# Performance work log

Hardware: AMD Instinct MI355X
Metric: run time of the kernel (lower is better)

The kernel has to match this reference:

```python
import jax, jax.numpy as jnp
import numpy as np

IMG = 1024.0            # image H = W
PRE_NMS, POST_NMS = 2000, 1000
NMS_THR, MIN_SZ = 0.7, 16.0
B = 16                  # batch of images


def _make_anchors():
    # Standard FPN anchor tiling: strides {4..64}, one scale per level, 3 ratios.
    strides = [4, 8, 16, 32, 64]
    scales = [32.0, 64.0, 128.0, 256.0, 512.0]
    ratios = [0.5, 1.0, 2.0]
    out = []
    for s, sc in zip(strides, scales):
        n = int(IMG) // s
        c = (np.arange(n, dtype=np.float32) + 0.5) * s
        xs, ys = np.meshgrid(c, c, indexing="xy")
        ctr = np.stack([xs.ravel(), ys.ravel()], -1)              # (n*n, 2) cx,cy
        wh = np.array([[sc * np.sqrt(1.0 / r), sc * np.sqrt(r)] for r in ratios],
                      dtype=np.float32)                           # (3, 2)
        b = np.concatenate([ctr[:, None, :] - wh[None] / 2,
                            ctr[:, None, :] + wh[None] / 2], -1)  # (n*n, 3, 4)
        out.append(b.reshape(-1, 4))
    return np.concatenate(out, 0).astype(np.float32)              # (261888, 4)


def setup_inputs() -> dict:
    key = jax.random.key(0)
    k1, k2 = jax.random.split(key)
    anchors = jnp.asarray(_make_anchors())
    A = anchors.shape[0]
    deltas = jax.random.normal(k1, (B, A, 4), dtype=jnp.float32) * 0.1
    scores = jax.random.uniform(k2, (B, A), dtype=jnp.float32)    # post-sigmoid objectness
    return {"anchors": anchors, "deltas": deltas, "scores": scores}


def _decode(anchors, deltas):
    # decode_boxes: deltas (tx,ty,tw,th) applied to anchors; dw/dh clamped at 4.0
    aw = anchors[:, 2] - anchors[:, 0]
    ah = anchors[:, 3] - anchors[:, 1]
    ax = anchors[:, 0] + 0.5 * aw
    ay = anchors[:, 1] + 0.5 * ah
    dx, dy = deltas[..., 0], deltas[..., 1]
    dw = jnp.minimum(deltas[..., 2], 4.0)
    dh = jnp.minimum(deltas[..., 3], 4.0)
    px = dx * aw + ax
    py = dy * ah + ay
    pw = jnp.exp(dw) * aw
    ph = jnp.exp(dh) * ah
    return jnp.stack([px - 0.5 * pw, py - 0.5 * ph,
                      px + 0.5 * pw, py + 0.5 * ph], -1)


def _box_iou(a, b):
    area_a = (a[:, 2] - a[:, 0]) * (a[:, 3] - a[:, 1])
    area_b = (b[:, 2] - b[:, 0]) * (b[:, 3] - b[:, 1])
    lt = jnp.maximum(a[:, None, :2], b[None, :, :2])
    rb = jnp.minimum(a[:, None, 2:], b[None, :, 2:])
    wh = jnp.clip(rb - lt, 0.0)
    inter = wh[..., 0] * wh[..., 1]
    return inter / (area_a[:, None] + area_b[None, :] - inter + 1e-6)


def _filter_one(props, s):
    # RegionProposalNetwork._filter: clip -> size filter -> topk(pre_nms) -> NMS -> post_nms
    x1 = jnp.clip(props[:, 0], 0.0, IMG)
    y1 = jnp.clip(props[:, 1], 0.0, IMG)
    x2 = jnp.clip(props[:, 2], 0.0, IMG)
    y2 = jnp.clip(props[:, 3], 0.0, IMG)
    valid = (x2 - x1 >= MIN_SZ) & (y2 - y1 >= MIN_SZ)
    ms = jnp.where(valid, s, -jnp.inf)                 # mask instead of boolean gather (jit)
    vals, idx = jax.lax.top_k(ms, PRE_NMS)            # sorted desc, as in scores.topk
    b = jnp.stack([x1, y1, x2, y2], -1)[idx]          # (PRE_NMS, 4)
    iou = _box_iou(b, b)                              # (PRE_NMS, PRE_NMS)
    later = jnp.arange(PRE_NMS)

    def body(i, keep):
        # suppress later boxes overlapping a still-kept box i (greedy NMS)
        sup = (iou[i] > NMS_THR) & keep[i] & (later > i)
        return keep & ~sup

    keep = jax.lax.fori_loop(0, PRE_NMS, body, jnp.ones(PRE_NMS, dtype=bool))
    fs = jnp.where(keep, vals, -jnp.inf)
    fv, fi = jax.lax.top_k(fs, POST_NMS)              # kept boxes, desc score order
    good = jnp.isfinite(fv)                           # padding mask for suppressed slots
    boxes = jnp.where(good[:, None], b[fi], 0.0)
    sc = jnp.where(good, fv, 0.0)
    return jnp.concatenate([boxes, sc[:, None]], -1)  # (POST_NMS, 5) = (x1,y1,x2,y2,score)


def reference(anchors, deltas, scores):
    props = _decode(anchors, deltas)                  # (B, A, 4)
    return jax.vmap(_filter_one)(props, scores)       # (B, POST_NMS, 5)
```

## Files before the change

kernel.cpp:

```cpp
#include <hip/hip_runtime.h>
#include <stdint.h>
#include <math.h>


#define IMGF 1024.0f
#define PRE_NMS 2000
#define POST_NMS 1000
#define NMS_THR 0.7f
#define MIN_SZ 16.0f
#define CAP 4096
#define SEL 2048
#define NW (SEL / 64)
#define CNT_STRIDE 32
#define KEY_NEGINF 0x007FFFFFu
#define MAXCHUNK 12

__device__ __forceinline__ uint32_t f2key(float f) {
  uint32_t u = __float_as_uint(f);
  return (u & 0x80000000u) ? ~u : (u | 0x80000000u);
}
__device__ __forceinline__ float key2f(uint32_t k) {
  uint32_t u = (k & 0x80000000u) ? (k & 0x7FFFFFFFu) : ~k;
  return __uint_as_float(u);
}

__device__ __forceinline__ unsigned long long readlane_u64(unsigned long long v,
                                                           int lane) {
  unsigned int lo = __builtin_amdgcn_readlane((unsigned int)v, lane);
  unsigned int hi = __builtin_amdgcn_readlane((unsigned int)(v >> 32), lane);
  return ((unsigned long long)hi << 32) | lo;
}

__device__ __forceinline__ float4 decode_clip(float4 anc, float4 dlt) {
  float aw = anc.z - anc.x;
  float ah = anc.w - anc.y;
  float ax = anc.x + 0.5f * aw;
  float ay = anc.y + 0.5f * ah;
  float dw = fminf(dlt.z, 4.0f);
  float dh = fminf(dlt.w, 4.0f);
  float px = dlt.x * aw + ax;
  float py = dlt.y * ah + ay;
  float pw = expf(dw) * aw;
  float ph = expf(dh) * ah;
  float x1 = px - 0.5f * pw, y1 = py - 0.5f * ph;
  float x2 = px + 0.5f * pw, y2 = py + 0.5f * ph;
  x1 = fminf(fmaxf(x1, 0.0f), IMGF);
  y1 = fminf(fmaxf(y1, 0.0f), IMGF);
  x2 = fminf(fmaxf(x2, 0.0f), IMGF);
  y2 = fminf(fmaxf(y2, 0.0f), IMGF);
  return make_float4(x1, y1, x2, y2);
}

__global__ void k_decode(const float4* __restrict__ anchors,
                         const float4* __restrict__ deltas,
                         const float* __restrict__ scores,
                         uint32_t* __restrict__ keys,
                         uint32_t* __restrict__ chist,
                         int A, int chunks) {
  int b = blockIdx.y;
  int t = threadIdx.x;
  int lane = t & 63;
  __shared__ uint32_t shist[256];
  shist[t] = 0;
  __syncthreads();
  int base_a = blockIdx.x * (chunks * 256);
  for (int c = 0; c < chunks; c++) {
    int a = base_a + c * 256 + t;
    bool inb = a < A;
    int ac = inb ? a : (A - 1);
    size_t i = (size_t)b * A + ac;
    float4 box = decode_clip(anchors[ac], deltas[i]);
    bool valid = (box.z - box.x >= MIN_SZ) && (box.w - box.y >= MIN_SZ);
    float ms = valid ? scores[i] : -INFINITY;
    uint32_t k = f2key(ms);
    if (inb) keys[i] = k;
    uint32_t bucket = k >> 24;
    bool fin = inb && (k != KEY_NEGINF);
    unsigned long long match = __ballot(fin);
#pragma unroll
    for (int bit = 0; bit < 8; bit++) {
      bool hb = (bucket >> bit) & 1;
      unsigned long long bb = __ballot(hb && fin);
      match &= hb ? bb : ~bb;
    }
    if (fin && (__ffsll((long long)match) - 1 == lane))
      atomicAdd(&shist[bucket], (uint32_t)__popcll(match));
  }
  __syncthreads();
  uint32_t v = shist[t];
  if (v) atomicAdd(&chist[b * 256 + t], v);
}

__global__ void k_coarse(const uint32_t* __restrict__ chist,
                         int* __restrict__ cbArr,
                         uint32_t* __restrict__ cumArr) {
  int b = blockIdx.x;
  int t = threadIdx.x;
  __shared__ uint32_t sA[256];
  sA[t] = chist[b * 256 + t];
  for (int d = 1; d < 256; d <<= 1) {
    __syncthreads();
    uint32_t v = sA[t] + ((t + d < 256) ? sA[t + d] : 0u);
    __syncthreads();
    sA[t] = v;
  }
  __syncthreads();
  if (t == 0 && sA[0] < PRE_NMS) {
    cbArr[b] = -1;
    cumArr[b] = 0;
  }
  uint32_t nxt = (t < 255) ? sA[t + 1] : 0u;
  if (sA[t] >= PRE_NMS && nxt < PRE_NMS) {
    cbArr[b] = t;
    cumArr[b] = nxt;
  }
}

__global__ void k_fine(const uint32_t* __restrict__ keys,
                       const int* __restrict__ cbArr,
                       uint32_t* __restrict__ fhist,
                       int A, int chunks) {
  int b = blockIdx.y;
  int t = threadIdx.x;
  int cb = cbArr[b];
  if (cb < 0) return;
  __shared__ uint32_t shist[256];
  shist[t] = 0;
  __syncthreads();
  int base_a = blockIdx.x * (chunks * 256);
  uint32_t cbu = (uint32_t)cb;
  for (int c = 0; c < chunks; c++) {
    int a = base_a + c * 256 + t;
    if (a >= A) break;
    uint32_t k = keys[(size_t)b * A + a];
    if ((k >> 24) == cbu && k != KEY_NEGINF)
      atomicAdd(&shist[(k >> 16) & 0xFFu], 1u);
  }
  __syncthreads();
  uint32_t v = shist[t];
  if (v) atomicAdd(&fhist[b * 256 + t], v);
}

__global__ void k_thresh(const uint32_t* __restrict__ fhist,
                         const int* __restrict__ cbArr,
                         const uint32_t* __restrict__ cumArr,
                         uint32_t* __restrict__ thresh,
                         uint32_t* __restrict__ cnts) {
  int b = blockIdx.x;
  int t = threadIdx.x;
  __shared__ uint32_t sA[256];
  if (t < 2) cnts[b * CNT_STRIDE + t] = 0;
  int cb = cbArr[b];
  if (cb < 0) {
    if (t == 0) thresh[b] = 0u;
    return;
  }
  uint32_t cumAbove = cumArr[b];
  sA[t] = fhist[b * 256 + t];
  for (int d = 1; d < 256; d <<= 1) {
    __syncthreads();
    uint32_t v = sA[t] + ((t + d < 256) ? sA[t + d] : 0u);
    __syncthreads();
    sA[t] = v;
  }
  __syncthreads();
  uint32_t nxt = (t < 255) ? sA[t + 1] : 0u;
  if (cumAbove + sA[t] >= PRE_NMS && cumAbove + nxt < PRE_NMS)
    thresh[b] = (uint32_t)((cb << 8) | t);
}

__global__ void k_gather(const uint32_t* __restrict__ keys,
                         const uint32_t* __restrict__ thresh,
                         uint32_t* __restrict__ cnts,
                         unsigned long long* __restrict__ cand_sort,
                         float4* __restrict__ sel_box,
                         float* __restrict__ sel_score,
                         int A, int chunks) {
  int b = blockIdx.y;
  int t = threadIdx.x;
  int lane = t & 63;
  int w = t >> 6;
  if (blockIdx.x < SEL / 256) {
    int r = blockIdx.x * 256 + t;
    sel_score[(size_t)b * SEL + r] = -INFINITY;
    sel_box[(size_t)b * SEL + r] = make_float4(0.0f, 0.0f, 0.0f, 0.0f);
  }
  __shared__ unsigned long long s_mA[MAXCHUNK * 4], s_mT[MAXCHUNK * 4];
  __shared__ uint32_t s_offA[MAXCHUNK * 4], s_offT[MAXCHUNK * 4];
  __shared__ uint32_t s_cA[MAXCHUNK * 4], s_cT[MAXCHUNK * 4];
  __shared__ uint32_t s_baseA, s_baseT;
  uint32_t beta = thresh[b];
  uint32_t kreg[MAXCHUNK];
  int base_a = blockIdx.x * (chunks * 256);
  for (int c = 0; c < chunks; c++) {
    int a = base_a + c * 256 + t;
    bool inb = a < A;
    uint32_t k = inb ? keys[(size_t)b * A + a] : KEY_NEGINF;
    kreg[c] = k;
    uint32_t bk = k >> 16;
    bool fin = (k != KEY_NEGINF);
    unsigned long long mA = __ballot(fin && (bk > beta));
    unsigned long long mT = __ballot(fin && (bk == beta));
    if (lane == 0) {
      s_mA[c * 4 + w] = mA;
      s_mT[c * 4 + w] = mT;
    }
  }
  __syncthreads();
  if (t < chunks * 4) {
    s_cA[t] = (uint32_t)__popcll(s_mA[t]);
    s_cT[t] = (uint32_t)__popcll(s_mT[t]);
  }
  __syncthreads();
  if (t == 0) {
    uint32_t accA = 0, accT = 0;
    for (int id = 0; id < chunks * 4; id++) {
      s_offA[id] = accA;
      accA += s_cA[id];
      s_offT[id] = accT;
      accT += s_cT[id];
    }
    s_baseA = accA ? atomicAdd(&cnts[b * CNT_STRIDE + 0], accA) : 0u;
    s_baseT = accT ? atomicAdd(&cnts[b * CNT_STRIDE + 1], accT) : 0u;
  }
  __syncthreads();
  uint32_t baseA = s_baseA, baseT = s_baseT;
  unsigned long long lower = ((unsigned long long)1 << lane) - 1;
  for (int c = 0; c < chunks; c++) {
    int id = c * 4 + w;
    unsigned long long mA = s_mA[id], mT = s_mT[id];
    bool above = (mA >> lane) & 1;
    bool tie = (mT >> lane) & 1;
    if (!(above || tie)) continue;
    int pos;
    if (above) {
      pos = (int)(baseA + s_offA[id] + (uint32_t)__popcll(mA & lower));
      if (pos >= PRE_NMS) continue;
    } else {
      pos = CAP - 1 - (int)(baseT + s_offT[id] + (uint32_t)__popcll(mT & lower));
      if (pos < PRE_NMS) continue;
    }
    int a = base_a + c * 256 + t;
    cand_sort[(size_t)b * CAP + pos] =
        ((unsigned long long)kreg[c] << 32) | (uint32_t)(~(uint32_t)a);
  }
}

__global__ void k_rank(const unsigned long long* __restrict__ cand_sort,
                       const uint32_t* __restrict__ cnts,
                       const float4* __restrict__ anchors,
                       const float4* __restrict__ deltas,
                       float4* __restrict__ sel_box,
                       float* __restrict__ sel_score, int A) {
  int b = blockIdx.y;
  int t = threadIdx.x;
  uint32_t c1 = cnts[b * CNT_STRIDE + 0];
  if (c1 > PRE_NMS) c1 = PRE_NMS;
  uint32_t c2 = cnts[b * CNT_STRIDE + 1];
  if (c2 > CAP - PRE_NMS) c2 = CAP - PRE_NMS;
  int loTie = CAP - (int)c2;
  int bs = blockIdx.x * 256;
  if (bs >= (int)c1 && bs + 256 <= loTie) return;
  int s = bs + t;
  bool live = (s < (int)c1) || (s >= loTie);
  unsigned long long myKey = live ? cand_sort[(size_t)b * CAP + s] : 0ull;
  __shared__ unsigned long long tile[256];
  int rank = 0;
  for (int ts = 0; ts < CAP; ts += 256) {
    if (ts >= (int)c1 && ts + 256 <= loTie) continue;
    int idx = ts + t;
    bool lv = (idx < (int)c1) || (idx >= loTie);
    __syncthreads();
    tile[t] = lv ? cand_sort[(size_t)b * CAP + idx] : 0ull;
    __syncthreads();
    if (live) {
#pragma unroll 8
      for (int j = 0; j < 256; j++) rank += (tile[j] > myKey) ? 1 : 0;
    }
  }
  if (live && rank < SEL) {
    uint32_t a = ~((uint32_t)myKey);
    float4 box = decode_clip(anchors[a], deltas[(size_t)b * A + a]);
    sel_score[(size_t)b * SEL + rank] = key2f((uint32_t)(myKey >> 32));
    sel_box[(size_t)b * SEL + rank] = box;
  }
}

__global__ void k_nmsmask(const float4* __restrict__ sel_box,
                          unsigned long long* __restrict__ mask,
                          unsigned long long* __restrict__ maskT) {
  int jb = blockIdx.x;
  int ib = blockIdx.y;
  int b = blockIdx.z;
  int t = threadIdx.x;
  int i = ib * 64 + t;
  if (jb < ib) {
    mask[((size_t)b * SEL + i) * NW + jb] = 0ull;
    return;
  }
  __shared__ float4 cb[64];
  __shared__ float careb[64];
  int j0 = jb * 64;
  float4 cbx = sel_box[(size_t)b * SEL + j0 + t];
  cb[t] = cbx;
  careb[t] = (cbx.z - cbx.x) * (cbx.w - cbx.y);
  __syncthreads();
  bool pad = (i >= PRE_NMS);
  if (pad && jb != ib) {
    mask[((size_t)b * SEL + i) * NW + jb] = 0ull;
    return;
  }
  float4 a = sel_box[(size_t)b * SEL + i];
  float area_a = (a.z - a.x) * (a.w - a.y);
  unsigned long long bits = 0ull;
  int jmax = min(64, PRE_NMS - j0);
  if (!pad) {
    for (int jj = 0; jj < jmax; jj++) {
      int j = j0 + jj;
      if (j <= i) continue;
      float4 bb = cb[jj];
      float ltx = fmaxf(a.x, bb.x), lty = fmaxf(a.y, bb.y);
      float rbx = fminf(a.z, bb.z), rby = fminf(a.w, bb.w);
      float w = fmaxf(rbx - ltx, 0.0f), hgt = fmaxf(rby - lty, 0.0f);
      float inter = w * hgt;
      float iou = inter / (area_a + careb[jj] - inter + 1e-6f);
      if (iou > NMS_THR) bits |= (1ull << jj);
    }
  }
  mask[((size_t)b * SEL + i) * NW + jb] = bits;
  if (jb == ib) {
    unsigned long long myT = 0ull;
#pragma unroll 1
    for (int jj = 0; jj < 64; jj++) {
      unsigned long long colw = __ballot((bits >> jj) & 1ull);
      if (t == jj) myT = colw;
    }
    maskT[(size_t)b * SEL + i] = myT;
  }
}

__global__ void __launch_bounds__(64, 1)
k_scanout(const float4* __restrict__ sel_box,
          const float* __restrict__ sel_score,
          const unsigned long long* __restrict__ mask,
          const unsigned long long* __restrict__ maskT,
          float* __restrict__ out) {
  int b = blockIdx.x;
  int t = threadIdx.x;
  int tw = t & 31;
  __shared__ uint32_t keptList[POST_NMS + 64];
  __shared__ unsigned long long tile[2][64 * NW];
  unsigned long long removed = 0ull;
  int kc = 0;
  const unsigned long long* mbase = mask + (size_t)b * SEL * NW;
  const unsigned long long* tbase = maskT + (size_t)b * SEL;
  const int lastChunk = (PRE_NMS - 1) / 64;
  int g = t >> 4;
  int cq = (t & 15) * 16;

  {
    const char* gb = (const char*)mbase;
#pragma unroll
    for (int k = 0; k < 16; k++) {
      const void* gp = gb + (size_t)(4 * k + g) * (NW * 8) + cq;
      __builtin_amdgcn_global_load_lds(
          (const __attribute__((address_space(1))) uint32_t*)gp,
          (__attribute__((address_space(3))) uint32_t*)&tile[0][(size_t)k * 128],
          16, 0, 0);
    }
  }
  unsigned long long colm = tbase[t];
  uint32_t scb = __float_as_uint(sel_score[(size_t)b * SEL + t]);

  for (int chunk = 0; chunk <= lastChunk; chunk++) {
    int cur = chunk & 1;
    unsigned long long colm_n = 0ull;
    uint32_t scb_n = 0xFF800000u;
    if (chunk < lastChunk) {
      const char* gb = (const char*)(mbase + (size_t)(chunk + 1) * 64 * NW);
#pragma unroll
      for (int k = 0; k < 16; k++) {
        const void* gp = gb + (size_t)(4 * k + g) * (NW * 8) + cq;
        __builtin_amdgcn_global_load_lds(
            (const __attribute__((address_space(1))) uint32_t*)gp,
            (__attribute__((address_space(3))) uint32_t*)
                &tile[cur ^ 1][(size_t)k * 128],
            16, 0, 0);
      }
      colm_n = tbase[(chunk + 1) * 64 + t];
      scb_n =
          __float_as_uint(sel_score[(size_t)b * SEL + (chunk + 1) * 64 + t]);
    }
    int rmax = PRE_NMS - chunk * 64;
    if (rmax > 64) rmax = 64;
    unsigned long long vb = __ballot(scb != 0xFF800000u);
    unsigned long long curw = readlane_u64(removed, chunk);
    unsigned long long range = (rmax >= 64) ? ~0ull : ((1ull << rmax) - 1ull);
    unsigned long long alive0 = ~curw & range;
    unsigned long long K = alive0;
    bool aliveb = (alive0 >> t) & 1ull;
#pragma unroll 1
    for (int it = 0; it < 64; ++it) {
      bool deadb = (colm & K) != 0ull;
      unsigned long long Kn = __ballot(aliveb && !deadb);
      if (Kn == K) break;
      K = Kn;
    }
    unsigned long long keptbits = K;
    unsigned long long kv = keptbits & vb;
    if ((kv >> t) & 1ull) {
      int rank = (int)__popcll(kv & ((1ull << t) - 1ull));
      keptList[kc + rank] = (uint32_t)(chunk * 64 + t);
    }
    kc += (int)__popcll(kv);
    if (kc >= POST_NMS) break;
    if (chunk == lastChunk) break;
    asm volatile("s_waitcnt vmcnt(18)" ::: "memory");
    __builtin_amdgcn_sched_barrier(0);
    uint32_t klo = (uint32_t)keptbits;
    uint32_t khi = (uint32_t)(keptbits >> 32);
#pragma unroll
    for (int j = 0; j < 32; j++) {
      unsigned long long mk =
          (unsigned long long)(-(long long)((klo >> j) & 1u));
      removed |= tile[cur][j * NW + tw] & mk;
    }
#pragma unroll
    for (int j = 0; j < 32; j++) {
      unsigned long long mk =
          (unsigned long long)(-(long long)((khi >> j) & 1u));
      removed |= tile[cur][(32 + j) * NW + tw] & mk;
    }
    __builtin_amdgcn_sched_barrier(0);
    colm = colm_n;
    scb = scb_n;
  }
  int kcc = kc < POST_NMS ? kc : POST_NMS;
  __syncthreads();
  for (int r = t; r < POST_NMS; r += 64) {
    float4 bx = make_float4(0.0f, 0.0f, 0.0f, 0.0f);
    float sc = 0.0f;
    if (r < kcc) {
      int i = (int)keptList[r];
      bx = sel_box[(size_t)b * SEL + i];
      sc = sel_score[(size_t)b * SEL + i];
    }
    float* o = out + ((size_t)b * POST_NMS + r) * 5;
    o[0] = bx.x;
    o[1] = bx.y;
    o[2] = bx.z;
    o[3] = bx.w;
    o[4] = sc;
  }
}

extern "C" void kernel_launch(void* const* d_in, const int* in_sizes, int n_in,
                              void* d_out, int out_size, void* d_ws, size_t ws_size,
                              hipStream_t stream) {
  const float* anchors = (const float*)d_in[0];
  const float* deltas = (const float*)d_in[1];
  const float* scores = (const float*)d_in[2];
  int A = in_sizes[0] / 4;
  int BA = in_sizes[2];
  int B = BA / A;
  float* out = (float*)d_out;

  char* ws = (char*)d_ws;
  size_t off = 0;
  uint32_t* keys = (uint32_t*)(ws + off);
  off += (size_t)BA * 4;
  uint32_t* chist = (uint32_t*)(ws + off);
  off += (size_t)B * 256 * 4;
  uint32_t* fhist = (uint32_t*)(ws + off);
  off += (size_t)B * 256 * 4;
  int* cbArr = (int*)(ws + off);
  off += (size_t)B * 4;
  uint32_t* cumArr = (uint32_t*)(ws + off);
  off += (size_t)B * 4;
  uint32_t* thresh = (uint32_t*)(ws + off);
  off += (size_t)B * 4;
  off = (off + 127) & ~(size_t)127;
  uint32_t* cnts = (uint32_t*)(ws + off);
  off += (size_t)B * CNT_STRIDE * 4;
  off = (off + 15) & ~(size_t)15;
  unsigned long long* cand_sort = (unsigned long long*)(ws + off);
  off += (size_t)B * CAP * 8;
  float4* sel_box = (float4*)(ws + off);
  off += (size_t)B * SEL * 16;
  float* sel_score = (float*)(ws + off);
  off += (size_t)B * SEL * 4;
  unsigned long long* mask = (unsigned long long*)(ws + off);
  off += (size_t)B * SEL * NW * 8;
  unsigned long long* maskT = (unsigned long long*)(ws + off);
  off += (size_t)B * SEL * 8;

  int chunks = (A % (256 * 11) == 0) ? 11 : 1;
  int bpb = (A + 256 * chunks - 1) / (256 * chunks);

  hipMemsetAsync(chist, 0, (size_t)B * 256 * 4 * 2, stream);
  k_decode<<<dim3(bpb, B), 256, 0, stream>>>((const float4*)anchors,
                                             (const float4*)deltas, scores,
                                             keys, chist, A, chunks);
  k_coarse<<<B, 256, 0, stream>>>(chist, cbArr, cumArr);
  k_fine<<<dim3(bpb, B), 256, 0, stream>>>(keys, cbArr, fhist, A, chunks);
  k_thresh<<<B, 256, 0, stream>>>(fhist, cbArr, cumArr, thresh, cnts);
  k_gather<<<dim3(bpb, B), 256, 0, stream>>>(keys, thresh, cnts, cand_sort,
                                             sel_box, sel_score, A, chunks);
  k_rank<<<dim3(CAP / 256, B), 256, 0, stream>>>(cand_sort, cnts,
                                                 (const float4*)anchors,
                                                 (const float4*)deltas,
                                                 sel_box, sel_score, A);
  k_nmsmask<<<dim3(NW, SEL / 64, B), 64, 0, stream>>>(sel_box, mask, maskT);
  k_scanout<<<B, 64, 0, stream>>>(sel_box, sel_score, mask, maskT, out);
}
```

Before: 288.8 us.

## Restructure NMS mask kernel into balanced row-block pairs with LDS-staged coalesced stores

The IoU mask kernel used to launch one 64-thread block per (row-block, column-block) tile, with half of those blocks only writing zeros. It now launches one 256-thread block per pair of row blocks (p and 31-p) so the triangular workload is balanced. Four wavefronts sweep the column blocks, prefetching the next column tile, and bits are staged in LDS before a coalesced write of whole mask rows. This cuts block count and launch overhead and improves store coalescing, but each block does more serial work and fewer blocks run concurrently.

```diff
diff --git a/kernel.cpp b/kernel.cpp
--- a/kernel.cpp
+++ b/kernel.cpp
@@ -286,56 +286,71 @@
   }
 }
 
-__global__ void k_nmsmask(const float4* __restrict__ sel_box,
-                          unsigned long long* __restrict__ mask,
-                          unsigned long long* __restrict__ maskT) {
-  int jb = blockIdx.x;
-  int ib = blockIdx.y;
-  int b = blockIdx.z;
-  int t = threadIdx.x;
-  int i = ib * 64 + t;
-  if (jb < ib) {
-    mask[((size_t)b * SEL + i) * NW + jb] = 0ull;
-    return;
-  }
-  __shared__ float4 cb[64];
-  __shared__ float careb[64];
-  int j0 = jb * 64;
-  float4 cbx = sel_box[(size_t)b * SEL + j0 + t];
-  cb[t] = cbx;
-  careb[t] = (cbx.z - cbx.x) * (cbx.w - cbx.y);
-  __syncthreads();
-  bool pad = (i >= PRE_NMS);
-  if (pad && jb != ib) {
-    mask[((size_t)b * SEL + i) * NW + jb] = 0ull;
-    return;
-  }
-  float4 a = sel_box[(size_t)b * SEL + i];
-  float area_a = (a.z - a.x) * (a.w - a.y);
-  unsigned long long bits = 0ull;
-  int jmax = min(64, PRE_NMS - j0);
-  if (!pad) {
-    for (int jj = 0; jj < jmax; jj++) {
-      int j = j0 + jj;
-      if (j <= i) continue;
-      float4 bb = cb[jj];
-      float ltx = fmaxf(a.x, bb.x), lty = fmaxf(a.y, bb.y);
-      float rbx = fminf(a.z, bb.z), rby = fminf(a.w, bb.w);
-      float w = fmaxf(rbx - ltx, 0.0f), hgt = fmaxf(rby - lty, 0.0f);
-      float inter = w * hgt;
-      float iou = inter / (area_a + careb[jj] - inter + 1e-6f);
-      if (iou > NMS_THR) bits |= (1ull << jj);
-    }
-  }
-  mask[((size_t)b * SEL + i) * NW + jb] = bits;
-  if (jb == ib) {
-    unsigned long long myT = 0ull;
+__global__ void __launch_bounds__(256)
+k_nmsmask(const float4* __restrict__ sel_box,
+          unsigned long long* __restrict__ mask,
+          unsigned long long* __restrict__ maskT) {
+  int p = blockIdx.x;
+  int b = blockIdx.y;
+  int t = threadIdx.x;
+  int lane = t & 63;
+  int w = t >> 6;
+  __shared__ float4 rowb[64];
+  __shared__ float rowarea[64];
+  __shared__ float4 colb[4][64];
+  __shared__ float colarea[4][64];
+  __shared__ unsigned long long bits_lds[64 * (NW + 1)];
+  for (int half = 0; half < 2; half++) {
+    int ib = half ? (31 - p) : p;
+    for (int k = t; k < 64 * (NW + 1); k += 256) bits_lds[k] = 0ull;
+    if (t < 64) {
+      float4 rb = sel_box[(size_t)b * SEL + ib * 64 + t];
+      rowb[t] = rb;
+      rowarea[t] = (rb.z - rb.x) * (rb.w - rb.y);
+    }
+    __syncthreads();
+    float4 abox = rowb[lane];
+    float area_a = rowarea[lane];
+    int i = ib * 64 + lane;
+    bool rowlive = (i < PRE_NMS);
+    int jb0 = ib + w;
+    float4 nb = make_float4(0.0f, 0.0f, 0.0f, 0.0f);
+    if (jb0 < NW) nb = sel_box[(size_t)b * SEL + jb0 * 64 + lane];
+    for (int jb = jb0; jb < NW; jb += 4) {
+      colb[w][lane] = nb;
+      colarea[w][lane] = (nb.z - nb.x) * (nb.w - nb.y);
+      if (jb + 4 < NW) nb = sel_box[(size_t)b * SEL + (jb + 4) * 64 + lane];
+      bool diag = (jb == ib);
+      unsigned long long bits = 0ull;
+      if (rowlive) {
+#pragma unroll 4
+        for (int jj = 0; jj < 64; jj++) {
+          if (diag && jj <= lane) continue;
+          float4 bb = colb[w][jj];
+          float ltx = fmaxf(abox.x, bb.x), lty = fmaxf(abox.y, bb.y);
+          float rbx = fminf(abox.z, bb.z), rby = fminf(abox.w, bb.w);
+          float ww = fmaxf(rbx - ltx, 0.0f), hh = fmaxf(rby - lty, 0.0f);
+          float inter = ww * hh;
+          float iou = inter / (area_a + colarea[w][jj] - inter + 1e-6f);
+          if (iou > NMS_THR) bits |= (1ull << jj);
+        }
+      }
+      bits_lds[lane * (NW + 1) + jb] = bits;
+      if (diag) {
+        unsigned long long myT = 0ull;
 #pragma unroll 1
-    for (int jj = 0; jj < 64; jj++) {
-      unsigned long long colw = __ballot((bits >> jj) & 1ull);
-      if (t == jj) myT = colw;
-    }
-    maskT[(size_t)b * SEL + i] = myT;
+        for (int jj = 0; jj < 64; jj++) {
+          unsigned long long colw = __ballot((bits >> jj) & 1ull);
+          if (lane == jj) myT = colw;
+        }
+        maskT[(size_t)b * SEL + (size_t)i] = myT;
+      }
+    }
+    __syncthreads();
+    size_t base = ((size_t)b * SEL + (size_t)ib * 64) * NW;
+    for (int k = t; k < 64 * NW; k += 256)
+      mask[base + k] = bits_lds[(k >> 5) * (NW + 1) + (k & 31)];
+    __syncthreads();
   }
 }
 
@@ -510,6 +525,6 @@
                                                  (const float4*)anchors,
                                                  (const float4*)deltas,
                                                  sel_box, sel_score, A);
-  k_nmsmask<<<dim3(NW, SEL / 64, B), 64, 0, stream>>>(sel_box, mask, maskT);
+  k_nmsmask<<<dim3(SEL / 128, B), 256, 0, stream>>>(sel_box, mask, maskT);
   k_scanout<<<B, 64, 0, stream>>>(sel_box, sel_score, mask, maskT, out);
 }
```

After: 326.2 us. +12.9%, slower.

## Store NMS mask column-block-major and skip lower-triangle mask writes

Applied to the files above, without the earlier changes.

The IoU suppression mask is now stored as [batch][column block][row], so each mask-kernel block writes 64 consecutive 64-bit words instead of words strided by the row pitch. Blocks below the diagonal return without writing zeros, and padded rows no longer take a separate early-exit path. The scan kernel loads and reads its tiles in the new orientation, with a rotated LDS index to spread bank accesses. It masks out the never-written lower-triangle words by block index, so it now depends on that masking being correct rather than on stored zeros.

```diff
diff --git a/kernel.cpp b/kernel.cpp
--- a/kernel.cpp
+++ b/kernel.cpp
@@ -291,13 +291,10 @@
                           unsigned long long* __restrict__ maskT) {
   int jb = blockIdx.x;
   int ib = blockIdx.y;
+  if (jb < ib) return;
   int b = blockIdx.z;
   int t = threadIdx.x;
   int i = ib * 64 + t;
-  if (jb < ib) {
-    mask[((size_t)b * SEL + i) * NW + jb] = 0ull;
-    return;
-  }
   __shared__ float4 cb[64];
   __shared__ float careb[64];
   int j0 = jb * 64;
@@ -305,19 +302,14 @@
   cb[t] = cbx;
   careb[t] = (cbx.z - cbx.x) * (cbx.w - cbx.y);
   __syncthreads();
-  bool pad = (i >= PRE_NMS);
-  if (pad && jb != ib) {
-    mask[((size_t)b * SEL + i) * NW + jb] = 0ull;
-    return;
-  }
   float4 a = sel_box[(size_t)b * SEL + i];
   float area_a = (a.z - a.x) * (a.w - a.y);
   unsigned long long bits = 0ull;
-  int jmax = min(64, PRE_NMS - j0);
-  if (!pad) {
+  if (i < PRE_NMS) {
+    bool diag = (jb == ib);
+    int jmax = min(64, PRE_NMS - j0);
     for (int jj = 0; jj < jmax; jj++) {
-      int j = j0 + jj;
-      if (j <= i) continue;
+      if (diag && jj <= t) continue;
       float4 bb = cb[jj];
       float ltx = fmaxf(a.x, bb.x), lty = fmaxf(a.y, bb.y);
       float rbx = fminf(a.z, bb.z), rby = fminf(a.w, bb.w);
@@ -327,7 +319,7 @@
       if (iou > NMS_THR) bits |= (1ull << jj);
     }
   }
-  mask[((size_t)b * SEL + i) * NW + jb] = bits;
+  mask[((size_t)b * NW + jb) * SEL + i] = bits;
   if (jb == ib) {
     unsigned long long myT = 0ull;
 #pragma unroll 1
@@ -352,20 +344,20 @@
   __shared__ unsigned long long tile[2][64 * NW];
   unsigned long long removed = 0ull;
   int kc = 0;
-  const unsigned long long* mbase = mask + (size_t)b * SEL * NW;
+  const unsigned long long* mb = mask + (size_t)b * NW * SEL;
   const unsigned long long* tbase = maskT + (size_t)b * SEL;
   const int lastChunk = (PRE_NMS - 1) / 64;
-  int g = t >> 4;
-  int cq = (t & 15) * 16;
+  int cjb = t >> 5;
+  int ro = (t & 31) * 2;
 
   {
-    const char* gb = (const char*)mbase;
 #pragma unroll
     for (int k = 0; k < 16; k++) {
-      const void* gp = gb + (size_t)(4 * k + g) * (NW * 8) + cq;
+      const unsigned long long* gp =
+          mb + ((size_t)(2 * k + cjb)) * SEL + ro;
       __builtin_amdgcn_global_load_lds(
           (const __attribute__((address_space(1))) uint32_t*)gp,
-          (__attribute__((address_space(3))) uint32_t*)&tile[0][(size_t)k * 128],
+          (__attribute__((address_space(3))) uint32_t*)&tile[0][k * 128],
           16, 0, 0);
     }
   }
@@ -377,14 +369,14 @@
     unsigned long long colm_n = 0ull;
     uint32_t scb_n = 0xFF800000u;
     if (chunk < lastChunk) {
-      const char* gb = (const char*)(mbase + (size_t)(chunk + 1) * 64 * NW);
 #pragma unroll
       for (int k = 0; k < 16; k++) {
-        const void* gp = gb + (size_t)(4 * k + g) * (NW * 8) + cq;
+        const unsigned long long* gp =
+            mb + ((size_t)(2 * k + cjb)) * SEL + (size_t)(chunk + 1) * 64 + ro;
         __builtin_amdgcn_global_load_lds(
             (const __attribute__((address_space(1))) uint32_t*)gp,
             (__attribute__((address_space(3))) uint32_t*)
-                &tile[cur ^ 1][(size_t)k * 128],
+                &tile[cur ^ 1][k * 128],
             16, 0, 0);
       }
       colm_n = tbase[(chunk + 1) * 64 + t];
@@ -417,20 +409,17 @@
     if (chunk == lastChunk) break;
     asm volatile("s_waitcnt vmcnt(18)" ::: "memory");
     __builtin_amdgcn_sched_barrier(0);
-    uint32_t klo = (uint32_t)keptbits;
-    uint32_t khi = (uint32_t)(keptbits >> 32);
+    unsigned long long acc = 0ull;
 #pragma unroll
-    for (int j = 0; j < 32; j++) {
+    for (int j = 0; j < 64; j++) {
+      int jr = (j + tw) & 63;
+      unsigned long long v = tile[cur][tw * 64 + jr];
       unsigned long long mk =
-          (unsigned long long)(-(long long)((klo >> j) & 1u));
-      removed |= tile[cur][j * NW + tw] & mk;
-    }
-#pragma unroll
-    for (int j = 0; j < 32; j++) {
-      unsigned long long mk =
-          (unsigned long long)(-(long long)((khi >> j) & 1u));
-      removed |= tile[cur][(32 + j) * NW + tw] & mk;
-    }
+          (unsigned long long)(-(long long)((keptbits >> jr) & 1ull));
+      acc |= v & mk;
+    }
+    unsigned long long wv = (tw >= chunk) ? ~0ull : 0ull;
+    removed |= acc & wv;
     __builtin_amdgcn_sched_barrier(0);
     colm = colm_n;
     scb = scb_n;
@@ -490,7 +479,7 @@
   float* sel_score = (float*)(ws + off);
   off += (size_t)B * SEL * 4;
   unsigned long long* mask = (unsigned long long*)(ws + off);
-  off += (size_t)B * SEL * NW * 8;
+  off += (size_t)B * NW * SEL * 8;
   unsigned long long* maskT = (unsigned long long*)(ws + off);
   off += (size_t)B * SEL * 8;
 
@@ -510,6 +499,6 @@
                                                  (const float4*)anchors,
                                                  (const float4*)deltas,
                                                  sel_box, sel_score, A);
-  k_nmsmask<<<dim3(NW, SEL / 64, B), 64, 0, stream>>>(sel_box, mask, maskT);
+  k_nmsmask<<<dim3(NW, NW, B), 64, 0, stream>>>(sel_box, mask, maskT);
   k_scanout<<<B, 64, 0, stream>>>(sel_box, sel_score, mask, maskT, out);
 }
```

Measured after the change: 286.9 us. No clear change (-0.7%).
